# Performance work log

Hardware: AMD Instinct MI355X
Metric: run time of the kernel (lower is better)

The kernel has to match this reference:

```python
import jax, jax.numpy as jnp
import numpy as np
import math

B, C, RES, N, H = 32, 32, 16, 16384, 64
G = RES ** 3
RATIO = 1.0


def _halton2(n):
    # 2-D Halton sequence (radical inverse, bases 2 and 3), shape (2, n)
    def radinv(idx, base):
        inv = np.zeros(n, dtype=np.float64)
        f = 1.0 / base
        i = idx.copy()
        while i.max() > 0:
            inv += f * (i % base)
            i //= base
            f /= base
        return inv
    idx = np.arange(1, n + 1)
    return np.stack([radinv(idx, 2), radinv(idx, 3)], axis=0).astype(np.float32)


def setup_inputs() -> dict:
    key = jax.random.key(0)
    ks = jax.random.split(key, 3)
    rng = np.random.default_rng(0)
    x = jax.random.normal(ks[0], (B, C, RES, RES, RES), dtype=jnp.float32)
    # density-driven counts: per-batch multinomial allocation summing exactly to N
    dens = rng.random((B, G)) ** 2
    probs = dens / dens.sum(axis=1, keepdims=True)
    counts = np.stack([rng.multinomial(N, probs[b]) for b in range(B)]).astype(np.int32)
    # grid offsets: ((meshgrid + 0.5) / res - 0.5).view(3, -1)  (normalize_ratio = 0.5)
    grid = np.stack(np.meshgrid(np.arange(RES), np.arange(RES), np.arange(RES), indexing='ij'), 0).astype(np.float32)
    grid_o = ((grid + 0.5) / RES - 0.5).reshape(3, -1)
    # Halton noise scaled: b_rnd * ratio - ratio/2, broadcast to batch
    b_rnd = _halton2(N) * RATIO - RATIO / 2.0
    b_rnd = np.broadcast_to(b_rnd[None], (B, 2, N)).copy()
    # pointwise generator MLP: (C+2) -> H -> 3
    W1 = jax.random.normal(ks[1], (H, C + 2), dtype=jnp.float32) * 0.05
    b1 = jnp.zeros((H,), dtype=jnp.float32)
    W2 = jax.random.normal(ks[2], (3, H), dtype=jnp.float32) * 0.05
    b2 = jnp.zeros((3,), dtype=jnp.float32)
    return {"x": x, "counts": jnp.asarray(counts), "b_rnd": jnp.asarray(b_rnd),
            "grid_o": jnp.asarray(grid_o), "W1": W1, "b1": b1, "W2": W2, "b2": b2}


def reference(x, counts, b_rnd, grid_o, W1, b1, W2, b2):
    b, c = x.shape[0], x.shape[1]
    n = b_rnd.shape[-1]
    xf = x.reshape(b, c, -1)                      # (b, c, G)
    # repeat_interleave(x[:, ind], counts[ind]) with fixed output size n:
    # output slot j maps to cell idx = searchsorted(cumsum(counts), j, 'right')
    cum = jnp.cumsum(counts, axis=1)              # (b, G)
    slots = jnp.arange(n)
    idx = jax.vmap(lambda cs: jnp.searchsorted(cs, slots, side='right'))(cum)  # (b, n)
    x_ind = jnp.take_along_axis(xf, idx[:, None, :], axis=2)                   # (b, c, n)
    o_ind = jnp.transpose(grid_o[:, idx], (1, 0, 2))                           # (b, 3, n)
    b_inp = jnp.concatenate([x_ind, b_rnd], axis=1)                            # (b, c+2, n)
    h = jax.nn.relu(jnp.einsum('hc,bcn->bhn', W1, b_inp) + b1[None, :, None])
    out = jnp.einsum('oh,bhn->bon', W2, h) + b2[None, :, None]                 # (b, 3, n)
    norm = jnp.linalg.norm(out, axis=1)                                        # (b, n)
    reg = jnp.clip(norm - math.sqrt(3.0) / RES, 0.0)
    return out + o_ind, reg
```

## Files before the change

### kernel.cpp

```cpp
#include <hip/hip_runtime.h>
#include <math.h>

constexpr int B_ = 32;
constexpr int C_ = 32;
constexpr int RES_ = 16;
constexpr int G_ = RES_ * RES_ * RES_;
constexpr int N_ = 16384;
constexpr int H_ = 64;
__device__ constexpr float REG_THR = 0.10825317547305483f;

__global__ __launch_bounds__(256) void scan_kernel(const int* __restrict__ counts,
                                                   int* __restrict__ cum) {
    const int b = blockIdx.x;
    const int* cb = counts + b * G_;
    int* ob = cum + b * G_;

    __shared__ int partials[256];
    const int t = threadIdx.x;
    const int base = t * 16;

    int local[16];
    int s = 0;
#pragma unroll
    for (int i = 0; i < 16; ++i) {
        s += cb[base + i];
        local[i] = s;
    }
    partials[t] = s;
    __syncthreads();

    for (int off = 1; off < 256; off <<= 1) {
        int v = (t >= off) ? partials[t - off] : 0;
        __syncthreads();
        partials[t] += v;
        __syncthreads();
    }
    const int prev = (t > 0) ? partials[t - 1] : 0;

#pragma unroll
    for (int i = 0; i < 16; ++i) ob[base + i] = prev + local[i];
}

__global__ __launch_bounds__(256) void mlp_kernel(
    const float* __restrict__ x, const float* __restrict__ b_rnd,
    const float* __restrict__ grid_o, const float* __restrict__ W1,
    const float* __restrict__ b1, const float* __restrict__ W2,
    const float* __restrict__ b2, const int* __restrict__ cum,
    float* __restrict__ out0, float* __restrict__ reg_out) {
    const int b = blockIdx.y;
    const int n = blockIdx.x * 256 + threadIdx.x;
    const int t = threadIdx.x;

    __shared__ int s_cum[G_];
    const int* cb = cum + b * G_;
#pragma unroll
    for (int i = 0; i < G_ / 256; ++i) s_cum[t + i * 256] = cb[t + i * 256];
    __syncthreads();

    int lo = 0, hi = G_ - 1;
#pragma unroll
    for (int it = 0; it < 12; ++it) {
        const int mid = (lo + hi) >> 1;
        if (s_cum[mid] > n) hi = mid; else lo = mid + 1;
        if (lo >= hi) { hi = lo; }
    }
    const int idx = lo;

    float inp[34];
    const float* xb = x + ((size_t)b * C_) * G_ + idx;
#pragma unroll
    for (int c = 0; c < C_; ++c) inp[c] = xb[(size_t)c * G_];
    inp[32] = b_rnd[((size_t)b * 2 + 0) * N_ + n];
    inp[33] = b_rnd[((size_t)b * 2 + 1) * N_ + n];

#pragma unroll
    for (int c = 0; c < 34; ++c) asm volatile("" : "+v"(inp[c]));

    float o0 = b2[0], o1 = b2[1], o2 = b2[2];
#pragma unroll 4
    for (int h = 0; h < H_; ++h) {
        float acc = b1[h];
        const float* w = W1 + h * 34;
#pragma unroll
        for (int c = 0; c < 34; ++c) acc = fmaf(w[c], inp[c], acc);
        acc = fmaxf(acc, 0.0f);
        o0 = fmaf(W2[0 * H_ + h], acc, o0);
        o1 = fmaf(W2[1 * H_ + h], acc, o1);
        o2 = fmaf(W2[2 * H_ + h], acc, o2);
    }

    const float nrm = sqrtf(o0 * o0 + o1 * o1 + o2 * o2);
    const float reg = fmaxf(nrm - REG_THR, 0.0f);

    o0 += grid_o[0 * G_ + idx];
    o1 += grid_o[1 * G_ + idx];
    o2 += grid_o[2 * G_ + idx];

    float* p = out0 + ((size_t)b * 3) * N_ + n;
    p[0]              = o0;
    p[N_]             = o1;
    p[2 * (size_t)N_] = o2;
    reg_out[(size_t)b * N_ + n] = reg;
}

extern "C" void kernel_launch(void* const* d_in, const int* in_sizes, int n_in,
                              void* d_out, int out_size, void* d_ws, size_t ws_size,
                              hipStream_t stream) {
    const float* x      = (const float*)d_in[0];
    const int*   counts = (const int*)  d_in[1];
    const float* b_rnd  = (const float*)d_in[2];
    const float* grid_o = (const float*)d_in[3];
    const float* W1     = (const float*)d_in[4];
    const float* b1     = (const float*)d_in[5];
    const float* W2     = (const float*)d_in[6];
    const float* b2     = (const float*)d_in[7];

    float* out  = (float*)d_out;
    float* rout = out + (size_t)B_ * 3 * N_;
    int*   cum  = (int*)d_ws;

    scan_kernel<<<B_, 256, 0, stream>>>(counts, cum);

    dim3 grid(N_ / 256, B_);
    mlp_kernel<<<grid, 256, 0, stream>>>(x, b_rnd, grid_o, W1, b1, W2, b2,
                                         cum, out, rout);
}
```

Measured before the change: 122.0 us.

## Precompute per-cell first-layer projection before gathering points

```diff
diff --git a/kernel.cpp b/kernel.cpp
--- a/kernel.cpp
+++ b/kernel.cpp
@@ -41,12 +41,41 @@
     for (int i = 0; i < 16; ++i) ob[base + i] = prev + local[i];
 }
 
-__global__ __launch_bounds__(256) void mlp_kernel(
-    const float* __restrict__ x, const float* __restrict__ b_rnd,
+__global__ __launch_bounds__(256) void hx_kernel(const float* __restrict__ x,
+                                                 const float* __restrict__ W1,
+                                                 const float* __restrict__ b1,
+                                                 float* __restrict__ hx) {
+    const int b = blockIdx.y;
+    const int cell = blockIdx.x * 256 + threadIdx.x;
+
+    const float* xb = x + ((size_t)b * C_) * G_ + cell;
+    float xv[C_];
+#pragma unroll
+    for (int c = 0; c < C_; ++c) xv[c] = xb[(size_t)c * G_];
+
+    float* ob = hx + ((size_t)b * G_ + cell) * H_;
+#pragma unroll 2
+    for (int hc = 0; hc < H_ / 4; ++hc) {
+        float a[4];
+#pragma unroll
+        for (int j = 0; j < 4; ++j) {
+            const int h = hc * 4 + j;
+            float acc = b1[h];
+            const float* w = W1 + h * 34;
+#pragma unroll
+            for (int c = 0; c < C_; ++c) acc = fmaf(w[c], xv[c], acc);
+            a[j] = acc;
+        }
+        *(float4*)(ob + hc * 4) = make_float4(a[0], a[1], a[2], a[3]);
+    }
+}
+
+__global__ __launch_bounds__(256) void point_kernel(
+    const float* __restrict__ hx, const float* __restrict__ b_rnd,
     const float* __restrict__ grid_o, const float* __restrict__ W1,
-    const float* __restrict__ b1, const float* __restrict__ W2,
-    const float* __restrict__ b2, const int* __restrict__ cum,
-    float* __restrict__ out0, float* __restrict__ reg_out) {
+    const float* __restrict__ W2, const float* __restrict__ b2,
+    const int* __restrict__ cum, float* __restrict__ out0,
+    float* __restrict__ reg_out) {
     const int b = blockIdx.y;
     const int n = blockIdx.x * 256 + threadIdx.x;
     const int t = threadIdx.x;
@@ -62,31 +91,30 @@
     for (int it = 0; it < 12; ++it) {
         const int mid = (lo + hi) >> 1;
         if (s_cum[mid] > n) hi = mid; else lo = mid + 1;
-        if (lo >= hi) { hi = lo; }
+        if (lo >= hi) hi = lo;
     }
     const int idx = lo;
 
-    float inp[34];
-    const float* xb = x + ((size_t)b * C_) * G_ + idx;
-#pragma unroll
-    for (int c = 0; c < C_; ++c) inp[c] = xb[(size_t)c * G_];
-    inp[32] = b_rnd[((size_t)b * 2 + 0) * N_ + n];
-    inp[33] = b_rnd[((size_t)b * 2 + 1) * N_ + n];
-
-#pragma unroll
-    for (int c = 0; c < 34; ++c) asm volatile("" : "+v"(inp[c]));
+    const float r0 = b_rnd[((size_t)b * 2 + 0) * N_ + n];
+    const float r1 = b_rnd[((size_t)b * 2 + 1) * N_ + n];
+    const float* hp = hx + ((size_t)b * G_ + idx) * H_;
 
     float o0 = b2[0], o1 = b2[1], o2 = b2[2];
 #pragma unroll 4
-    for (int h = 0; h < H_; ++h) {
-        float acc = b1[h];
-        const float* w = W1 + h * 34;
+    for (int hc = 0; hc < H_ / 4; ++hc) {
+        const float4 v = *(const float4*)(hp + hc * 4);
+        const float vv[4] = {v.x, v.y, v.z, v.w};
 #pragma unroll
-        for (int c = 0; c < 34; ++c) acc = fmaf(w[c], inp[c], acc);
-        acc = fmaxf(acc, 0.0f);
-        o0 = fmaf(W2[0 * H_ + h], acc, o0);
-        o1 = fmaf(W2[1 * H_ + h], acc, o1);
-        o2 = fmaf(W2[2 * H_ + h], acc, o2);
+        for (int j = 0; j < 4; ++j) {
+            const int h = hc * 4 + j;
+            float hv = vv[j];
+            hv = fmaf(W1[h * 34 + 32], r0, hv);
+            hv = fmaf(W1[h * 34 + 33], r1, hv);
+            hv = fmaxf(hv, 0.0f);
+            o0 = fmaf(W2[0 * H_ + h], hv, o0);
+            o1 = fmaf(W2[1 * H_ + h], hv, o1);
+            o2 = fmaf(W2[2 * H_ + h], hv, o2);
+        }
     }
 
     const float nrm = sqrtf(o0 * o0 + o1 * o1 + o2 * o2);
@@ -117,11 +145,16 @@
 
     float* out  = (float*)d_out;
     float* rout = out + (size_t)B_ * 3 * N_;
-    int*   cum  = (int*)d_ws;
+
+    int*   cum = (int*)d_ws;
+    float* hx  = (float*)((char*)d_ws + (size_t)B_ * G_ * sizeof(int));
 
     scan_kernel<<<B_, 256, 0, stream>>>(counts, cum);
 
-    dim3 grid(N_ / 256, B_);
-    mlp_kernel<<<grid, 256, 0, stream>>>(x, b_rnd, grid_o, W1, b1, W2, b2,
-                                         cum, out, rout);
+    dim3 gridA(G_ / 256, B_);
+    hx_kernel<<<gridA, 256, 0, stream>>>(x, W1, b1, hx);
+
+    dim3 gridB(N_ / 256, B_);
+    point_kernel<<<gridB, 256, 0, stream>>>(hx, b_rnd, grid_o, W1, W2, b2,
+                                            cum, out, rout);
 }
```

New measurement: 153.9 us. +26.2%, slower.

## Precompute per-cell hidden projections and iterate over points per cell tile

Applied to the files above, without the earlier changes.

```diff
diff --git a/kernel.cpp b/kernel.cpp
--- a/kernel.cpp
+++ b/kernel.cpp
@@ -41,66 +41,99 @@
     for (int i = 0; i < 16; ++i) ob[base + i] = prev + local[i];
 }
 
-__global__ __launch_bounds__(256) void mlp_kernel(
-    const float* __restrict__ x, const float* __restrict__ b_rnd,
-    const float* __restrict__ grid_o, const float* __restrict__ W1,
+constexpr int TCELL = 64;
+constexpr int PAD = H_ + 1;
+constexpr int WROW = 36;
+
+__global__ __launch_bounds__(256) void fused_kernel(
+    const float* __restrict__ x, const int* __restrict__ cum,
+    const float* __restrict__ b_rnd, const float* __restrict__ W1,
     const float* __restrict__ b1, const float* __restrict__ W2,
-    const float* __restrict__ b2, const int* __restrict__ cum,
-    float* __restrict__ out0, float* __restrict__ reg_out) {
+    const float* __restrict__ b2, float* __restrict__ out0,
+    float* __restrict__ reg_out) {
     const int b = blockIdx.y;
-    const int n = blockIdx.x * 256 + threadIdx.x;
+    const int c0 = blockIdx.x * TCELL;
     const int t = threadIdx.x;
+    const int cell_l = t & 63;
+    const int hh = __builtin_amdgcn_readfirstlane((t >> 6) * 16);
 
-    __shared__ int s_cum[G_];
-    const int* cb = cum + b * G_;
+    __shared__ float s_w1[H_ * WROW];
+    __shared__ float s_w2[3 * H_];
+    __shared__ float s_hx[TCELL * PAD];
+    __shared__ int s_cum[TCELL + 1];
+
+    for (int i = t; i < H_ * 34; i += 256) {
+        const int r = i / 34;
+        const int c = i - r * 34;
+        s_w1[r * WROW + c] = W1[i];
+    }
+    if (t < H_) s_w1[t * WROW + 34] = b1[t];
+    if (t < 3 * H_) s_w2[t] = W2[t];
+    if (t < TCELL + 1) {
+        const int g = c0 + t - 1;
+        s_cum[t] = (g >= 0) ? cum[b * G_ + g] : 0;
+    }
+
+    const float* xb = x + ((size_t)b * C_) * G_ + c0 + cell_l;
+    float xv[C_];
 #pragma unroll
-    for (int i = 0; i < G_ / 256; ++i) s_cum[t + i * 256] = cb[t + i * 256];
+    for (int c = 0; c < C_; ++c) xv[c] = xb[(size_t)c * G_];
     __syncthreads();
 
-    int lo = 0, hi = G_ - 1;
+    float* row = s_hx + cell_l * PAD + hh;
+#pragma unroll 4
+    for (int j = 0; j < 16; ++j) {
+        const float* w = s_w1 + (hh + j) * WROW;
+        float acc = w[34];
 #pragma unroll
-    for (int it = 0; it < 12; ++it) {
-        const int mid = (lo + hi) >> 1;
-        if (s_cum[mid] > n) hi = mid; else lo = mid + 1;
-        if (lo >= hi) { hi = lo; }
+        for (int c = 0; c < C_; ++c) acc = fmaf(w[c], xv[c], acc);
+        row[j] = acc;
     }
-    const int idx = lo;
+    const float b20 = b2[0], b21 = b2[1], b22 = b2[2];
+    __syncthreads();
 
-    float inp[34];
-    const float* xb = x + ((size_t)b * C_) * G_ + idx;
+    const int p_start = s_cum[0];
+    const int p_end = s_cum[TCELL];
+
+    for (int p = p_start + t; p < p_end; p += 256) {
+        int lo = 0, hi = TCELL - 1;
 #pragma unroll
-    for (int c = 0; c < C_; ++c) inp[c] = xb[(size_t)c * G_];
-    inp[32] = b_rnd[((size_t)b * 2 + 0) * N_ + n];
-    inp[33] = b_rnd[((size_t)b * 2 + 1) * N_ + n];
+        for (int it = 0; it < 6; ++it) {
+            const int mid = (lo + hi) >> 1;
+            if (s_cum[1 + mid] > p) hi = mid; else lo = mid + 1;
+        }
+        const int ci = lo;
+        const int idx = c0 + ci;
 
-#pragma unroll
-    for (int c = 0; c < 34; ++c) asm volatile("" : "+v"(inp[c]));
+        const float r0 = b_rnd[((size_t)b * 2 + 0) * N_ + p];
+        const float r1 = b_rnd[((size_t)b * 2 + 1) * N_ + p];
+        const float* hp = s_hx + ci * PAD;
 
-    float o0 = b2[0], o1 = b2[1], o2 = b2[2];
-#pragma unroll 4
-    for (int h = 0; h < H_; ++h) {
-        float acc = b1[h];
-        const float* w = W1 + h * 34;
-#pragma unroll
-        for (int c = 0; c < 34; ++c) acc = fmaf(w[c], inp[c], acc);
-        acc = fmaxf(acc, 0.0f);
-        o0 = fmaf(W2[0 * H_ + h], acc, o0);
-        o1 = fmaf(W2[1 * H_ + h], acc, o1);
-        o2 = fmaf(W2[2 * H_ + h], acc, o2);
+        float o0 = b20, o1 = b21, o2 = b22;
+#pragma unroll 8
+        for (int h = 0; h < H_; ++h) {
+            float hv = hp[h];
+            hv = fmaf(s_w1[h * WROW + 32], r0, hv);
+            hv = fmaf(s_w1[h * WROW + 33], r1, hv);
+            hv = fmaxf(hv, 0.0f);
+            o0 = fmaf(s_w2[h], hv, o0);
+            o1 = fmaf(s_w2[H_ + h], hv, o1);
+            o2 = fmaf(s_w2[2 * H_ + h], hv, o2);
+        }
+
+        const float nrm = sqrtf(o0 * o0 + o1 * o1 + o2 * o2);
+        const float reg = fmaxf(nrm - REG_THR, 0.0f);
+
+        o0 += (float)((idx >> 8) & 15) * 0.0625f - 0.46875f;
+        o1 += (float)((idx >> 4) & 15) * 0.0625f - 0.46875f;
+        o2 += (float)(idx & 15) * 0.0625f - 0.46875f;
+
+        float* op = out0 + ((size_t)b * 3) * N_ + p;
+        op[0]              = o0;
+        op[N_]             = o1;
+        op[2 * (size_t)N_] = o2;
+        reg_out[(size_t)b * N_ + p] = reg;
     }
-
-    const float nrm = sqrtf(o0 * o0 + o1 * o1 + o2 * o2);
-    const float reg = fmaxf(nrm - REG_THR, 0.0f);
-
-    o0 += grid_o[0 * G_ + idx];
-    o1 += grid_o[1 * G_ + idx];
-    o2 += grid_o[2 * G_ + idx];
-
-    float* p = out0 + ((size_t)b * 3) * N_ + n;
-    p[0]              = o0;
-    p[N_]             = o1;
-    p[2 * (size_t)N_] = o2;
-    reg_out[(size_t)b * N_ + n] = reg;
 }
 
 extern "C" void kernel_launch(void* const* d_in, const int* in_sizes, int n_in,
@@ -109,7 +142,6 @@
     const float* x      = (const float*)d_in[0];
     const int*   counts = (const int*)  d_in[1];
     const float* b_rnd  = (const float*)d_in[2];
-    const float* grid_o = (const float*)d_in[3];
     const float* W1     = (const float*)d_in[4];
     const float* b1     = (const float*)d_in[5];
     const float* W2     = (const float*)d_in[6];
@@ -117,11 +149,12 @@
 
     float* out  = (float*)d_out;
     float* rout = out + (size_t)B_ * 3 * N_;
-    int*   cum  = (int*)d_ws;
+
+    int* cum = (int*)d_ws;
 
     scan_kernel<<<B_, 256, 0, stream>>>(counts, cum);
 
-    dim3 grid(N_ / 256, B_);
-    mlp_kernel<<<grid, 256, 0, stream>>>(x, b_rnd, grid_o, W1, b1, W2, b2,
-                                         cum, out, rout);
+    dim3 grid(G_ / TCELL, B_);
+    fused_kernel<<<grid, 256, 0, stream>>>(x, cum, b_rnd, W1, b1, W2, b2,
+                                           out, rout);
 }
```

Measured after the change: 112.6 us. -7.7%, faster.
